# Kernel tuning notes

Hardware: AMD Instinct MI355X
Metric: run time of the kernel (lower is better)

The kernel has to match this reference:

```python
import jax, jax.numpy as jnp
import numpy as np

B, T, IN, OUT = 32, 128, 512, 512
N, Wd, R, H = 128, 64, 4, 512      # memory slots, word size, read heads, controller size
EPS = 1e-6
IFACE = R * Wd + R + Wd + 1 + Wd + Wd + R + 1 + 1 + 3 * R  # DNC interface vector size


def setup_inputs() -> dict:
    key = jax.random.key(0)
    ks = jax.random.split(key, 6)
    s = jnp.float32(0.05)
    lstm_in = IN + R * Wd
    return {
        "input_sequence": jax.random.normal(ks[0], (B, T, IN), jnp.float32),
        "Wx": jax.random.normal(ks[1], (lstm_in, 4 * H), jnp.float32) * s,
        "Wh": jax.random.normal(ks[2], (H, 4 * H), jnp.float32) * s,
        "b_lstm": jnp.zeros((4 * H,), jnp.float32),
        "W_iface": jax.random.normal(ks[3], (H, IFACE), jnp.float32) * s,
        "b_iface": jnp.zeros((IFACE,), jnp.float32),
        "W_out": jax.random.normal(ks[4], (R * Wd + H, OUT), jnp.float32) * s,
        "b_out": jnp.zeros((OUT,), jnp.float32),
    }


def _alloc(u):
    """DNC allocation weighting for one example. u: [N] usage in [0,1]."""
    phi = jnp.argsort(u)                      # ascending usage (data-dependent gather)
    su = u[phi]
    cp = jnp.cumprod(su)
    cp_excl = jnp.concatenate([jnp.ones((1,), su.dtype), cp[:-1]])
    a_sorted = (1.0 - su) * cp_excl
    return jnp.zeros_like(u).at[phi].set(a_sorted)  # scatter back to original order


def _content(M, keys, beta):
    """Cosine content addressing. M: [B,N,W], keys: [B,K,W], beta: [B,K] -> [B,K,N]."""
    Mn = M / (jnp.linalg.norm(M, axis=-1, keepdims=True) + EPS)
    kn = keys / (jnp.linalg.norm(keys, axis=-1, keepdims=True) + EPS)
    sim = jnp.einsum('bnw,bkw->bkn', Mn, kn)
    return jax.nn.softmax(beta[..., None] * sim, axis=-1)


def _dnc_forward(input_sequence, Wx, Wh, b_lstm, W_iface, b_iface, W_out, b_out):
    eye = 1.0 - jnp.eye(N, dtype=jnp.float32)

    def step(carry, x_t):
        h, c, M, usage, link, prec, ww, wr, reads = carry
        # --- LSTM controller ---
        z = jnp.concatenate([x_t, reads], -1) @ Wx + h @ Wh + b_lstm
        i_g, f_g, g_g, o_g = jnp.split(z, 4, axis=-1)
        c_n = jax.nn.sigmoid(f_g) * c + jax.nn.sigmoid(i_g) * jnp.tanh(g_g)
        h_n = jax.nn.sigmoid(o_g) * jnp.tanh(c_n)
        # --- interface vector ---
        v = h_n @ W_iface + b_iface
        o = [0]
        def take(n):
            out = v[:, o[0]:o[0] + n]; o[0] += n; return out
        read_keys = take(R * Wd).reshape(B, R, Wd)
        read_beta = 1.0 + jax.nn.softplus(take(R))
        write_key = take(Wd).reshape(B, 1, Wd)
        write_beta = 1.0 + jax.nn.softplus(take(1))
        erase = jax.nn.sigmoid(take(Wd))
        write_vec = take(Wd)
        free = jax.nn.sigmoid(take(R))
        alloc_g = jax.nn.sigmoid(take(1))
        write_g = jax.nn.sigmoid(take(1))
        modes = jax.nn.softmax(take(3 * R).reshape(B, R, 3), axis=-1)
        # --- usage & allocation ---
        retention = jnp.prod(1.0 - free[:, :, None] * wr, axis=1)          # [B,N]
        usage_n = (usage + ww - usage * ww) * retention
        a = jax.vmap(_alloc)(usage_n)
        # --- write ---
        cw = _content(M, write_key, write_beta)[:, 0, :]                    # [B,N]
        ww_n = write_g * (alloc_g * a + (1.0 - alloc_g) * cw)
        M_n = M * (1.0 - ww_n[:, :, None] * erase[:, None, :]) + ww_n[:, :, None] * write_vec[:, None, :]
        # --- temporal link ---
        link_n = ((1.0 - ww_n[:, :, None] - ww_n[:, None, :]) * link
                  + ww_n[:, :, None] * prec[:, None, :]) * eye
        prec_n = (1.0 - ww_n.sum(-1, keepdims=True)) * prec + ww_n
        # --- read ---
        fw = jnp.einsum('bij,brj->bri', link_n, wr)
        bw = jnp.einsum('bji,brj->bri', link_n, wr)
        cr = _content(M_n, read_keys, read_beta)
        wr_n = modes[:, :, 0:1] * bw + modes[:, :, 1:2] * cr + modes[:, :, 2:3] * fw
        reads_n = jnp.einsum('brn,bnw->brw', wr_n, M_n).reshape(B, R * Wd)
        # --- output projection ---
        out = jnp.concatenate([reads_n, h_n], -1) @ W_out + b_out
        return (h_n, c_n, M_n, usage_n, link_n, prec_n, ww_n, wr_n, reads_n), out

    f32 = jnp.float32
    init = (jnp.zeros((B, H), f32), jnp.zeros((B, H), f32),
            jnp.zeros((B, N, Wd), f32), jnp.zeros((B, N), f32),
            jnp.zeros((B, N, N), f32), jnp.zeros((B, N), f32),
            jnp.zeros((B, N), f32), jnp.zeros((B, R, N), f32),
            jnp.zeros((B, R * Wd), f32))
    _, outs = jax.lax.scan(step, init, jnp.swapaxes(input_sequence, 0, 1))
    return jnp.swapaxes(outs, 0, 1)  # [B, T, OUT]


def reference(input_sequence, Wx, Wh, b_lstm, W_iface, b_iface, W_out, b_out):
    return _dnc_forward(input_sequence, Wx, Wh, b_lstm, W_iface, b_iface, W_out, b_out)
```

## Files before the change

kernel.cpp:

```cpp
#include <hip/hip_runtime.h>
#include <math.h>

#define TT 128
#define ZD 2048
#define IFC 471
#define EPSF 1e-6f
#define MST 66
#define LST 130
#define NBLK 256
#define UHT 24640
#define VHT 15424

#define FSP 16
#define NFLAGS 8192

#define D4(a,b) ((a).x*(b).x + (a).y*(b).y + (a).z*(b).z + (a).w*(b).w)

__device__ __forceinline__ float sig_(float x){ return 1.f/(1.f+expf(-x)); }
__device__ __forceinline__ float sp_(float x){ return fmaxf(x,0.f)+log1pf(expf(-fabsf(x))); }

__device__ __forceinline__ void st1(float* p, float v){
  unsigned u; __builtin_memcpy(&u,&v,4);
  __hip_atomic_store((unsigned*)p, u, __ATOMIC_RELAXED, __HIP_MEMORY_SCOPE_AGENT);
}
__device__ __forceinline__ void st2(float* p, float2 v){
  unsigned long long u; __builtin_memcpy(&u,&v,8);
  __hip_atomic_store((unsigned long long*)p, u, __ATOMIC_RELAXED, __HIP_MEMORY_SCOPE_AGENT);
}

__device__ __forceinline__ void arrive(unsigned* f, unsigned gen){
  __syncthreads();
  if (threadIdx.x == 0)
    __hip_atomic_store(f, gen, __ATOMIC_RELAXED, __HIP_MEMORY_SCOPE_AGENT);
}
__device__ __forceinline__ void wait_ge(const unsigned* f, int n, unsigned gen){
  if (threadIdx.x < 64){
    for (int i = threadIdx.x; i < n; i += 64){
      const unsigned* p = f + (size_t)i*FSP;
      if (__hip_atomic_load(p, __ATOMIC_RELAXED, __HIP_MEMORY_SCOPE_AGENT) >= gen) continue;
      int spins = 0; bool done = false;
      while (spins < 64){
        if (__hip_atomic_load(p, __ATOMIC_RELAXED, __HIP_MEMORY_SCOPE_AGENT) >= gen){ done = true; break; }
        __builtin_amdgcn_s_sleep(1); ++spins;
      }
      if (!done){
        while (__hip_atomic_load(p, __ATOMIC_RELAXED, __HIP_MEMORY_SCOPE_AGENT) < gen)
          __builtin_amdgcn_s_sleep(2);
      }
    }
  }
  __syncthreads();
}

__device__ __forceinline__ unsigned bf16rne(float f){
  unsigned u; __builtin_memcpy(&u,&f,4);
  return (u + 0x7fffu + ((u>>16)&1u)) >> 16;
}
__device__ __forceinline__ float bflo(unsigned w){
  unsigned u = w << 16; float f; __builtin_memcpy(&f,&u,4); return f;
}
__device__ __forceinline__ float bfhi(unsigned w){
  unsigned u = w & 0xffff0000u; float f; __builtin_memcpy(&f,&u,4); return f;
}

__global__ __launch_bounds__(256) void gemm_bias(
    const float* __restrict__ A, const float* __restrict__ B,
    const float* __restrict__ bias, float* __restrict__ C,
    int Nc, int K)
{
  __shared__ float As[16][68];
  __shared__ float Bs[16][68];
  const int tid = threadIdx.x;
  const int bx = blockIdx.x, by = blockIdx.y;
  const int tx = tid & 15, ty = tid >> 4;
  const int am = tid >> 2, ak = (tid & 3) * 4;
  const int bk = tid >> 4, bn = (tid & 15) * 4;
  float acc[4][4] = {};
  const float* Ap = A + (size_t)(by*64+am)*K + ak;
  const float* Bp = B + (size_t)bk*Nc + bx*64 + bn;
  for (int k0 = 0; k0 < K; k0 += 16) {
    float4 av = *(const float4*)Ap; Ap += 16;
    float4 bv = *(const float4*)Bp; Bp += (size_t)16*Nc;
    As[ak+0][am]=av.x; As[ak+1][am]=av.y; As[ak+2][am]=av.z; As[ak+3][am]=av.w;
    *(float4*)&Bs[bk][bn] = bv;
    __syncthreads();
#pragma unroll
    for (int kk = 0; kk < 16; ++kk) {
      float4 a4 = *(const float4*)&As[kk][ty*4];
      float4 b4 = *(const float4*)&Bs[kk][tx*4];
      acc[0][0]+=a4.x*b4.x; acc[0][1]+=a4.x*b4.y; acc[0][2]+=a4.x*b4.z; acc[0][3]+=a4.x*b4.w;
      acc[1][0]+=a4.y*b4.x; acc[1][1]+=a4.y*b4.y; acc[1][2]+=a4.y*b4.z; acc[1][3]+=a4.y*b4.w;
      acc[2][0]+=a4.z*b4.x; acc[2][1]+=a4.z*b4.y; acc[2][2]+=a4.z*b4.z; acc[2][3]+=a4.z*b4.w;
      acc[3][0]+=a4.w*b4.x; acc[3][1]+=a4.w*b4.y; acc[3][2]+=a4.w*b4.z; acc[3][3]+=a4.w*b4.w;
    }
    __syncthreads();
  }
  float4 bb = *(const float4*)(bias + bx*64 + tx*4);
#pragma unroll
  for (int i = 0; i < 4; ++i) {
    float4 o;
    o.x = acc[i][0]+bb.x; o.y = acc[i][1]+bb.y; o.z = acc[i][2]+bb.z; o.w = acc[i][3]+bb.w;
    *(float4*)(C + (size_t)(by*64+ty*4+i)*Nc + bx*64 + tx*4) = o;
  }
}

__global__ __launch_bounds__(256) void gemm_out(
    const float* __restrict__ A, const float* __restrict__ B,
    const float* __restrict__ bias, float* __restrict__ C)
{
  __shared__ float As[16][68];
  __shared__ float Bs[16][68];
  const int tid = threadIdx.x;
  const int bx = blockIdx.x, by = blockIdx.y;
  const int tx = tid & 15, ty = tid >> 4;
  const int am = tid >> 2, ak = (tid & 3) * 4;
  const int bk = tid >> 4, bn = (tid & 15) * 4;
  float acc[4][4] = {};
  const int arow = by*64 + am;
  const float* Ap = A + (size_t)(arow >> 5)*UHT + (size_t)(arow & 31)*768 + ak;
  const float* Bp = B + (size_t)bk*512 + bx*64 + bn;
  for (int k0 = 0; k0 < 768; k0 += 16) {
    float4 av = *(const float4*)Ap; Ap += 16;
    float4 bv = *(const float4*)Bp; Bp += (size_t)16*512;
    As[ak+0][am]=av.x; As[ak+1][am]=av.y; As[ak+2][am]=av.z; As[ak+3][am]=av.w;
    *(float4*)&Bs[bk][bn] = bv;
    __syncthreads();
#pragma unroll
    for (int kk = 0; kk < 16; ++kk) {
      float4 a4 = *(const float4*)&As[kk][ty*4];
      float4 b4 = *(const float4*)&Bs[kk][tx*4];
      acc[0][0]+=a4.x*b4.x; acc[0][1]+=a4.x*b4.y; acc[0][2]+=a4.x*b4.z; acc[0][3]+=a4.x*b4.w;
      acc[1][0]+=a4.y*b4.x; acc[1][1]+=a4.y*b4.y; acc[1][2]+=a4.y*b4.z; acc[1][3]+=a4.y*b4.w;
      acc[2][0]+=a4.z*b4.x; acc[2][1]+=a4.z*b4.y; acc[2][2]+=a4.z*b4.z; acc[2][3]+=a4.z*b4.w;
      acc[3][0]+=a4.w*b4.x; acc[3][1]+=a4.w*b4.y; acc[3][2]+=a4.w*b4.z; acc[3][3]+=a4.w*b4.w;
    }
    __syncthreads();
  }
  float4 bb = *(const float4*)(bias + bx*64 + tx*4);
#pragma unroll
  for (int i = 0; i < 4; ++i) {
    int row = by*64 + ty*4 + i;
    int crow = (row & 31)*128 + (row >> 5);
    float4 o;
    o.x = acc[i][0]+bb.x; o.y = acc[i][1]+bb.y; o.z = acc[i][2]+bb.z; o.w = acc[i][3]+bb.w;
    *(float4*)(C + (size_t)crow*512 + bx*64 + tx*4) = o;
  }
}

#define SL_L    0
#define SL_M    16640
#define SL_V    25088
#define SL_WR   25568
#define SL_FW   26080
#define SL_BW   26592
#define SL_CR   27104
#define SL_USG  27616
#define SL_PRC  27744
#define SL_WW   27872
#define SL_SU   28000
#define SL_CPX  28128
#define SL_MN   28256
#define SL_SW   28384
#define SL_CW   28512
#define SL_RNK  28640
#define SL_MSC  28768
#define SL_ER   28832
#define SL_WV   28896
#define SL_TOT  28960

#define CWI_U  29564
#define CUS_F  34004
#define CZH_F  37092
#define CCS_F  37396
#define CTOT_F 37548

__global__ void init_flags(unsigned* flags) {
  int idx = blockIdx.x*1024 + threadIdx.x;
  if (idx < NFLAGS)
    __hip_atomic_store(&flags[idx], 0u, __ATOMIC_RELAXED, __HIP_MEMORY_SCOPE_AGENT);
}

__global__ __launch_bounds__(1024) void dnc_coop(
    const float* __restrict__ Xproj, const float* __restrict__ Wx,
    const float* __restrict__ Wh, const float* __restrict__ Wif,
    const float* __restrict__ bif,
    float* __restrict__ Uh, float* __restrict__ Vh,
    unsigned* __restrict__ flags)
{
  const int blk = blockIdx.x, tid = threadIdx.x;
  extern __shared__ float sm[];
  const int g = blk & 7;
  const int role = blk >> 3;
  unsigned* FHg = flags + (size_t)g*64*FSP;
  unsigned* FVg = FHg + 28*FSP;
  unsigned* FRg = FHg + 56*FSP;

  if (role < 4) {
    const int eg = g*4 + role;
    float* L   = sm + SL_L;   float* Ms  = sm + SL_M;
    float* v   = sm + SL_V;   float* wr  = sm + SL_WR;
    float* fw  = sm + SL_FW;  float* bw  = sm + SL_BW;
    float* cr  = sm + SL_CR;  float* usg = sm + SL_USG;
    float* prc = sm + SL_PRC; float* ww  = sm + SL_WW;
    float* su  = sm + SL_SU;  float* cpx = sm + SL_CPX;
    float* Mn  = sm + SL_MN;  float* swv = sm + SL_SW;
    float* cw  = sm + SL_CW;  int*   rnk = (int*)(sm + SL_RNK);
    float* msc = sm + SL_MSC; float* er_ = sm + SL_ER; float* wv_ = sm + SL_WV;

    for (int i = tid; i < SL_TOT; i += 1024) sm[i] = 0.f;
    __syncthreads();

    for (int t = 0; t < TT; ++t) {
      wait_ge(FVg, 28, t+1);
      if (tid < IFC) v[tid] = Vh[(size_t)t*VHT + eg*480 + tid];
      __syncthreads();
      if (tid < 128) {
        float ret = 1.f;
#pragma unroll
        for (int r = 0; r < 4; ++r) { float fr = sig_(v[453+r]); ret *= 1.f - fr*wr[r*128+tid]; }
        float u = usg[tid], w_ = ww[tid];
        usg[tid] = (u + w_ - u*w_) * ret;
      } else if (tid < 256) {
        int n = tid - 128; float nk = 0.f, dot = 0.f;
#pragma unroll
        for (int w = 0; w < 64; w += 2) {
          float2 k2 = *(float2*)&v[260+w];
          float2 m2 = *(float2*)&Ms[n*MST+w];
          nk += k2.x*k2.x + k2.y*k2.y; dot += m2.x*k2.x + m2.y*k2.y;
        }
        float beta = 1.f + sp_(v[324]);
        swv[n] = beta * dot / ((Mn[n]+EPSF)*(sqrtf(nk)+EPSF));
      } else if (tid < 260) {
        int r = tid - 256; float s = 0.f;
#pragma unroll
        for (int w = 0; w < 64; w += 4) { float4 k4 = *(float4*)&v[r*64+w]; s += D4(k4,k4); }
        msc[1+r] = sqrtf(s);
      } else if (tid == 260) {
        for (int r = 0; r < 4; ++r) {
          float a0 = v[459+r*3], a1 = v[459+r*3+1], a2 = v[459+r*3+2];
          float mx = fmaxf(a0, fmaxf(a1, a2));
          float e0 = expf(a0-mx), e1 = expf(a1-mx), e2 = expf(a2-mx);
          float dn = e0+e1+e2;
          msc[8+r*3] = e0/dn; msc[8+r*3+1] = e1/dn; msc[8+r*3+2] = e2/dn;
        }
      } else if (tid >= 640 && tid < 704) { int w = tid-640; er_[w] = sig_(v[325+w]); }
      else if (tid >= 704 && tid < 768) { int w = tid-704; wv_[w] = v[389+w]; }
      __syncthreads();
      if (tid < 128) {
        float ui = usg[tid]; int rk = 0;
#pragma unroll
        for (int j = 0; j < 128; j += 4) {
          float4 u4 = *(float4*)&usg[j];
          rk += (u4.x < ui || (u4.x == ui && (j+0) < tid)) ? 1 : 0;
          rk += (u4.y < ui || (u4.y == ui && (j+1) < tid)) ? 1 : 0;
          rk += (u4.z < ui || (u4.z == ui && (j+2) < tid)) ? 1 : 0;
          rk += (u4.w < ui || (u4.w == ui && (j+3) < tid)) ? 1 : 0;
        }
        rnk[tid] = rk; su[rk] = ui;
      } else if (tid < 192) {
        int l = tid - 128;
        float s1 = swv[l], s2 = swv[l+64];
        float m = fmaxf(s1, s2);
#pragma unroll
        for (int o = 32; o > 0; o >>= 1) m = fmaxf(m, __shfl_xor(m, o));
        float e1 = expf(s1-m), e2 = expf(s2-m);
        float dn = e1 + e2;
#pragma unroll
        for (int o = 32; o > 0; o >>= 1) dn += __shfl_xor(dn, o);
        cw[l] = e1/dn; cw[l+64] = e2/dn;
      }
      __syncthreads();
      if (tid < 64) {
        float a0 = su[2*tid], a1 = su[2*tid+1];
        float p = a0*a1, sc = p;
#pragma unroll
        for (int off = 1; off < 64; off <<= 1) {
          float o = __shfl_up(sc, off);
          if ((int)tid >= off) sc *= o;
        }
        float ex = __shfl_up(sc, 1);
        if (tid == 0) ex = 1.f;
        cpx[2*tid] = ex;
        cpx[2*tid+1] = ex*a0;
        float ag = sig_(v[457]), wg = sig_(v[458]);
#pragma unroll
        for (int q = 0; q < 2; ++q) {
          int n = 2*tid + q;
          float a_i = (1.f - usg[n]) * cpx[rnk[n]];
          ww[n] = wg * (ag*a_i + (1.f-ag)*cw[n]);
        }
      }
      __syncthreads();
      {
        int n = tid >> 3, q = tid & 7;
        float wwn = ww[n];
        int w8 = q*8;
#pragma unroll
        for (int gq = 0; gq < 4; ++gq) {
          int w = w8 + gq*2;
          float2 m = *(float2*)&Ms[n*MST+w];
          float2 e2 = *(float2*)&er_[w];
          float2 v2 = *(float2*)&wv_[w];
          m.x = m.x*(1.f - wwn*e2.x) + wwn*v2.x;
          m.y = m.y*(1.f - wwn*e2.y) + wwn*v2.y;
          *(float2*)&Ms[n*MST+w] = m;
        }
        int j16 = q*16;
#pragma unroll
        for (int gq = 0; gq < 8; ++gq) {
          int j = j16 + gq*2;
          float2 lv = *(float2*)&L[n*LST + j];
          float2 p2 = *(float2*)&prc[j];
          float2 w2 = *(float2*)&ww[j];
          lv.x = (1.f - wwn - w2.x)*lv.x + wwn*p2.x;
          lv.y = (1.f - wwn - w2.y)*lv.y + wwn*p2.y;
          int d = n - j;
          if (d == 0) lv.x = 0.f;
          if (d == 1) lv.y = 0.f;
          *(float2*)&L[n*LST + j] = lv;
        }
      }
      __syncthreads();
      if (tid < 64) {
        float s = ww[tid] + ww[tid+64];
#pragma unroll
        for (int o = 32; o > 0; o >>= 1) s += __shfl_xor(s, o);
        if (tid == 0) msc[0] = s;
      } else if (tid < 192) {
        int n = tid - 64; float s = 0.f;
#pragma unroll
        for (int w = 0; w < 64; w += 2) { float2 m = *(float2*)&Ms[n*MST+w]; s += m.x*m.x + m.y*m.y; }
        Mn[n] = sqrtf(s);
      }
      __syncthreads();
      if (tid < 256) {
        int half = tid >> 7, t2 = tid & 127;
        int i0 = (t2 >> 2) * 4, sg = t2 & 3;
        float4 av[4] = {{0,0,0,0},{0,0,0,0},{0,0,0,0},{0,0,0,0}};
        if (half == 0) {
#pragma unroll
          for (int m = 0; m < 8; ++m) {
            int j = sg*4 + m*16;
            float4 w0 = *(float4*)&wr[0*128+j];
            float4 w1 = *(float4*)&wr[1*128+j];
            float4 w2 = *(float4*)&wr[2*128+j];
            float4 w3 = *(float4*)&wr[3*128+j];
#pragma unroll
            for (int k = 0; k < 4; ++k) {
              float2 la = *(float2*)&L[(i0+k)*LST+j];
              float2 lb = *(float2*)&L[(i0+k)*LST+j+2];
              float dv0 = la.x*w0.x + la.y*w0.y + lb.x*w0.z + lb.y*w0.w;
              float dv1 = la.x*w1.x + la.y*w1.y + lb.x*w1.z + lb.y*w1.w;
              float dv2 = la.x*w2.x + la.y*w2.y + lb.x*w2.z + lb.y*w2.w;
              float dv3 = la.x*w3.x + la.y*w3.y + lb.x*w3.z + lb.y*w3.w;
              if (k == 0){ av[0].x+=dv0; av[1].x+=dv1; av[2].x+=dv2; av[3].x+=dv3; }
              if (k == 1){ av[0].y+=dv0; av[1].y+=dv1; av[2].y+=dv2; av[3].y+=dv3; }
              if (k == 2){ av[0].z+=dv0; av[1].z+=dv1; av[2].z+=dv2; av[3].z+=dv3; }
              if (k == 3){ av[0].w+=dv0; av[1].w+=dv1; av[2].w+=dv2; av[3].w+=dv3; }
            }
          }
        } else {
#pragma unroll
          for (int m = 0; m < 32; ++m) {
            int j = sg + m*4;
            float2 la = *(float2*)&L[j*LST + i0];
            float2 lb = *(float2*)&L[j*LST + i0 + 2];
            float w0 = wr[j], w1 = wr[128+j], w2 = wr[256+j], w3 = wr[384+j];
            av[0].x+=w0*la.x; av[0].y+=w0*la.y; av[0].z+=w0*lb.x; av[0].w+=w0*lb.y;
            av[1].x+=w1*la.x; av[1].y+=w1*la.y; av[1].z+=w1*lb.x; av[1].w+=w1*lb.y;
            av[2].x+=w2*la.x; av[2].y+=w2*la.y; av[2].z+=w2*lb.x; av[2].w+=w2*lb.y;
            av[3].x+=w3*la.x; av[3].y+=w3*la.y; av[3].z+=w3*lb.x; av[3].w+=w3*lb.y;
          }
        }
#pragma unroll
        for (int r = 0; r < 4; ++r) {
          av[r].x += __shfl_xor(av[r].x,1); av[r].x += __shfl_xor(av[r].x,2);
          av[r].y += __shfl_xor(av[r].y,1); av[r].y += __shfl_xor(av[r].y,2);
          av[r].z += __shfl_xor(av[r].z,1); av[r].z += __shfl_xor(av[r].z,2);
          av[r].w += __shfl_xor(av[r].w,1); av[r].w += __shfl_xor(av[r].w,2);
        }
        if (sg == 0) {
          float* dst = half ? bw : fw;
#pragma unroll
          for (int r = 0; r < 4; ++r) {
            dst[r*128 + i0+0] = av[r].x; dst[r*128 + i0+1] = av[r].y;
            dst[r*128 + i0+2] = av[r].z; dst[r*128 + i0+3] = av[r].w;
          }
        }
      } else if (tid < 384) {
        int n = tid - 256;
        prc[n] = (1.f - msc[0])*prc[n] + ww[n];
      } else if (tid >= 512) {
        int r = (tid >> 7) & 3, n = tid & 127;
        float dot = 0.f;
#pragma unroll
        for (int w = 0; w < 64; w += 2) {
          float2 m2 = *(float2*)&Ms[n*MST+w];
          float2 k2 = *(float2*)&v[r*64+w];
          dot += m2.x*k2.x + m2.y*k2.y;
        }
        float beta = 1.f + sp_(v[256+r]);
        cr[r*128+n] = beta * dot / ((Mn[n]+EPSF)*(msc[1+r]+EPSF));
      }
      __syncthreads();
      if (tid < 256) {
        int r = tid >> 6, l = tid & 63;
        float s1 = cr[r*128+l], s2 = cr[r*128+l+64];
        float m = fmaxf(s1, s2);
#pragma unroll
        for (int o = 32; o > 0; o >>= 1) m = fmaxf(m, __shfl_xor(m, o));
        float e1 = expf(s1-m), e2 = expf(s2-m);
        float dn = e1 + e2;
#pragma unroll
        for (int o = 32; o > 0; o >>= 1) dn += __shfl_xor(dn, o);
        float m0 = msc[8+r*3], m1 = msc[8+r*3+1], m2 = msc[8+r*3+2];
        wr[r*128+l]    = m0*bw[r*128+l]    + m1*(e1/dn) + m2*fw[r*128+l];
        wr[r*128+l+64] = m0*bw[r*128+l+64] + m1*(e2/dn) + m2*fw[r*128+l+64];
      }
      __syncthreads();
      if (tid < 512) {
        int r = tid >> 7, t2 = tid & 127;
        int w0 = (t2 >> 3) * 4, ns = t2 & 7;
        float4 a = {0,0,0,0};
#pragma unroll
        for (int m = 0; m < 16; ++m) {
          int n = ns + m*8;
          float2 ma = *(float2*)&Ms[n*MST + w0];
          float2 mb = *(float2*)&Ms[n*MST + w0 + 2];
          float wv = wr[r*128 + n];
          a.x += wv*ma.x; a.y += wv*ma.y; a.z += wv*mb.x; a.w += wv*mb.y;
        }
        a.x += __shfl_xor(a.x,1); a.x += __shfl_xor(a.x,2); a.x += __shfl_xor(a.x,4);
        a.y += __shfl_xor(a.y,1); a.y += __shfl_xor(a.y,2); a.y += __shfl_xor(a.y,4);
        a.z += __shfl_xor(a.z,1); a.z += __shfl_xor(a.z,2); a.z += __shfl_xor(a.z,4);
        a.w += __shfl_xor(a.w,1); a.w += __shfl_xor(a.w,2); a.w += __shfl_xor(a.w,4);
        if (ns == 0) {
          int o = r*64 + w0;
          float2 lo = {a.x, a.y}, hi = {a.z, a.w};
          st2(&Uh[(size_t)t*UHT + eg*768 + o], lo);
          st2(&Uh[(size_t)t*UHT + eg*768 + o + 2], hi);
        }
      }
      arrive(&FRg[role*FSP], t+1);
    }
  } else {
    const int c = role - 4;
    const int egB = g*4;
    const int d0 = (512*c)/28, d1 = (512*(c+1))/28, Dd = d1-d0, NJ = 4*Dd;
    const int v0 = (471*c)/28, v1 = (471*(c+1))/28, JV = v1-v0;
    unsigned* Wzu = (unsigned*)sm;
    unsigned* Wiu = (unsigned*)sm + CWI_U;
    float* us  = sm + CUS_F;
    float* zh  = sm + CZH_F;
    float* cst = sm + CCS_F;

    for (int idx = tid; idx < NJ*384; idx += 1024) {
      int j = idx/384, p = idx - j*384, k = 2*p;
      int q = j/Dd, di = j - q*Dd, gc = q*512 + d0 + di;
      float w0 = (k < 256) ? Wx[(size_t)(512+k)*ZD + gc] : Wh[(size_t)(k-256)*ZD + gc];
      float w1 = (k+1 < 256) ? Wx[(size_t)(513+k)*ZD + gc] : Wh[(size_t)(k-255)*ZD + gc];
      Wzu[j*389 + p] = bf16rne(w0) | (bf16rne(w1) << 16);
    }
    for (int idx = tid; idx < JV*256; idx += 1024) {
      int j = idx/256, p = idx - j*256, k = 2*p, gc = v0 + j;
      float w0 = Wif[(size_t)k*IFC + gc];
      float w1 = Wif[(size_t)(k+1)*IFC + gc];
      Wiu[j*261 + p] = bf16rne(w0) | (bf16rne(w1) << 16);
    }
    if (tid < 76) cst[tid] = 0.f;
    if (tid < 4*NJ) {
      int e = tid/NJ, j = tid - e*NJ;
      int q = j/Dd, di = j - q*Dd, gc = q*512 + d0 + di;
      zh[e*76 + j] = Xproj[((size_t)(egB+e)*TT + 0)*ZD + gc];
    }
    __syncthreads();
    if (tid < 4*Dd) {
      int e = tid/Dd, di = tid - e*Dd;
      float zi = zh[e*76 + di], zg = zh[e*76 + 2*Dd + di], zo = zh[e*76 + 3*Dd + di];
      float cn = sig_(zi)*tanhf(zg);
      float hn = sig_(zo)*tanhf(cn);
      cst[tid] = cn;
      st1(&Uh[(size_t)0*UHT + (egB + e)*768 + 256 + d0 + di], hn);
    }
    arrive(&FHg[c*FSP], 1);

    for (int t = 0; t < TT; ++t) {
      float xpre = 0.f; int pe = 0, pj = 0;
      if (t+1 < TT && tid < 4*NJ) {
        pe = tid/NJ; pj = tid - pe*NJ;
        int q = pj/Dd, di = pj - q*Dd, gc = q*512 + d0 + di;
        xpre = Xproj[((size_t)(egB+pe)*TT + t+1)*ZD + gc];
      }
      wait_ge(FHg, 28, t+1);
      if (tid < 512) {
        int e = tid >> 7, f4 = (tid & 127) * 4;
        *(float4*)&us[e*772 + 256 + f4] =
            *(const float4*)&Uh[(size_t)t*UHT + (egB+e)*768 + 256 + f4];
      }
      if (t+1 < TT && tid < 4*NJ) {
        zh[pe*76 + pj] = xpre;
      }
      __syncthreads();
      if (tid < 544) {
        int g8 = tid >> 3, ks = tid & 7;
        int e = g8/17, j = g8 - e*17;
        if (j < JV) {
          float acc = 0.f;
#pragma unroll 4
          for (int m = 0; m < 32; ++m) {
            int p = m*8 + ks;
            float2 hv = *(const float2*)&us[e*772 + 256 + 2*p];
            unsigned wu = Wiu[j*261 + p];
            acc += hv.x*bflo(wu) + hv.y*bfhi(wu);
          }
          acc += __shfl_xor(acc,1); acc += __shfl_xor(acc,2); acc += __shfl_xor(acc,4);
          if (ks == 0) {
            int col = v0 + j;
            st1(&Vh[(size_t)t*VHT + (egB+e)*480 + col], bif[col] + acc);
          }
        }
      }
      arrive(&FVg[c*FSP], t+1);
      if (t+1 < TT) {
        if (tid < 608) {
          int q2 = tid >> 1, ks = tid & 1;
          int e = q2/76, j = q2 - e*76;
          if (j < NJ) {
            float acc = 0.f;
#pragma unroll 4
            for (int m = 0; m < 128; ++m) {
              int pp = m*2 + ks;
              float2 hv = *(const float2*)&us[e*772 + 256 + 2*pp];
              unsigned wu = Wzu[j*389 + 128 + pp];
              acc += hv.x*bflo(wu) + hv.y*bfhi(wu);
            }
            acc += __shfl_xor(acc,1);
            if (ks == 0) zh[e*76 + j] += acc;
          }
        }
        wait_ge(FRg, 4, t+1);
        if (tid < 256) {
          int e = tid >> 6, f4 = (tid & 63) * 4;
          *(float4*)&us[e*772 + f4] =
              *(const float4*)&Uh[(size_t)t*UHT + (egB+e)*768 + f4];
        }
        __syncthreads();
        if (tid < 608) {
          int q2 = tid >> 1, ks = tid & 1;
          int e = q2/76, j = q2 - e*76;
          if (j < NJ) {
            float acc = 0.f;
#pragma unroll 4
            for (int m = 0; m < 64; ++m) {
              int pp = m*2 + ks;
              float2 rv = *(const float2*)&us[e*772 + 2*pp];
              unsigned wu = Wzu[j*389 + pp];
              acc += rv.x*bflo(wu) + rv.y*bfhi(wu);
            }
            acc += __shfl_xor(acc,1);
            if (ks == 0) zh[e*76 + j] += acc;
          }
        }
        __syncthreads();
        if (tid < 4*Dd) {
          int e = tid/Dd, di = tid - e*Dd;
          float zi = zh[e*76 + di],      zf = zh[e*76 + Dd + di];
          float zg = zh[e*76 + 2*Dd+di], zo = zh[e*76 + 3*Dd + di];
          float cn = sig_(zf)*cst[tid] + sig_(zi)*tanhf(zg);
          float hn = sig_(zo)*tanhf(cn);
          cst[tid] = cn;
          st1(&Uh[(size_t)(t+1)*UHT + (egB+e)*768 + 256 + d0 + di], hn);
        }
        arrive(&FHg[c*FSP], t+2);
      }
    }
  }
}

extern "C" void kernel_launch(void* const* d_in, const int* in_sizes, int n_in,
                              void* d_out, int out_size, void* d_ws, size_t ws_size,
                              hipStream_t stream) {
  const float* x   = (const float*)d_in[0];
  const float* Wx  = (const float*)d_in[1];
  const float* Wh  = (const float*)d_in[2];
  const float* bl  = (const float*)d_in[3];
  const float* Wif = (const float*)d_in[4];
  const float* bif = (const float*)d_in[5];
  const float* Wo  = (const float*)d_in[6];
  const float* bo  = (const float*)d_in[7];
  float* out = (float*)d_out;

  unsigned* fl = (unsigned*)d_ws;
  float* Xp = (float*)(fl + NFLAGS);
  float* Uh = Xp + (size_t)4096*2048;
  float* Vh = Uh + (size_t)TT*UHT;

  gemm_bias<<<dim3(2048/64, 4096/64), dim3(256), 0, stream>>>(x, Wx, bl, Xp, 2048, 512);

  init_flags<<<dim3(8), dim3(1024), 0, stream>>>(fl);

  const int smem_bytes = CTOT_F * 4;
  (void)hipFuncSetAttribute((const void*)dnc_coop, hipFuncAttributeMaxDynamicSharedMemorySize, smem_bytes);
  void* args[] = { (void*)&Xp, (void*)&Wx, (void*)&Wh, (void*)&Wif, (void*)&bif,
                   (void*)&Uh, (void*)&Vh, (void*)&fl };
  (void)hipLaunchCooperativeKernel((void*)dnc_coop, dim3(NBLK), dim3(1024), args,
                                   (unsigned int)smem_bytes, stream);

  gemm_out<<<dim3(512/64, 4096/64), dim3(256), 0, stream>>>(Uh, Wo, bo, out);
}
```

Measured before the change: 4.112 ms.

## Fuse interface projection into LSTM step via split-K partial sums

Each controller block now computes its slice of h right after the LSTM cell and immediately multiplies it by the matching rows of W_iface, writing split-K partial interface vectors. The memory blocks sum the 28 partials plus bias. This removes one full grid-sync round (waiting for all h before computing the interface) from the critical path per timestep. The cost is 28x more global reads on the memory-side blocks and a Vpart buffer that is reused across timesteps, which relies on the flag ordering to avoid overwriting partials that have not yet been read.

```diff
diff --git a/kernel.cpp b/kernel.cpp
--- a/kernel.cpp
+++ b/kernel.cpp
@@ -9,7 +9,6 @@
 #define LST 130
 #define NBLK 256
 #define UHT 24640
-#define VHT 15424
 
 #define FSP 16
 #define NFLAGS 8192
@@ -26,6 +25,10 @@
 __device__ __forceinline__ void st2(float* p, float2 v){
   unsigned long long u; __builtin_memcpy(&u,&v,8);
   __hip_atomic_store((unsigned long long*)p, u, __ATOMIC_RELAXED, __HIP_MEMORY_SCOPE_AGENT);
+}
+__device__ __forceinline__ float ld1(const float* p){
+  unsigned u = __hip_atomic_load((const unsigned*)p, __ATOMIC_RELAXED, __HIP_MEMORY_SCOPE_AGENT);
+  float f; __builtin_memcpy(&f,&u,4); return f;
 }
 
 __device__ __forceinline__ void arrive(unsigned* f, unsigned gen){
@@ -167,12 +170,18 @@
 #define SL_ER   28832
 #define SL_WV   28896
 #define SL_TOT  28960
-
-#define CWI_U  29564
-#define CUS_F  34004
-#define CZH_F  37092
-#define CCS_F  37396
-#define CTOT_F 37548
+#define SL_BIF  28960
+
+#define CWR_U  29564
+#define CUS_F  34067
+#define CZH_F  37155
+#define CCS_F  37459
+#define CHS_F  37539
+#define CTOT_F 37619
+
+#define VPE 480
+#define VPC (4*VPE)
+#define VPG (28*VPC)
 
 __global__ void init_flags(unsigned* flags) {
   int idx = blockIdx.x*1024 + threadIdx.x;
@@ -184,7 +193,7 @@
     const float* __restrict__ Xproj, const float* __restrict__ Wx,
     const float* __restrict__ Wh, const float* __restrict__ Wif,
     const float* __restrict__ bif,
-    float* __restrict__ Uh, float* __restrict__ Vh,
+    float* __restrict__ Uh, float* __restrict__ Vpart,
     unsigned* __restrict__ flags)
 {
   const int blk = blockIdx.x, tid = threadIdx.x;
@@ -206,13 +215,22 @@
     float* Mn  = sm + SL_MN;  float* swv = sm + SL_SW;
     float* cw  = sm + SL_CW;  int*   rnk = (int*)(sm + SL_RNK);
     float* msc = sm + SL_MSC; float* er_ = sm + SL_ER; float* wv_ = sm + SL_WV;
+    float* bifs= sm + SL_BIF;
+    const float* Vp = Vpart + (size_t)g*VPG + (size_t)role*VPE;
 
     for (int i = tid; i < SL_TOT; i += 1024) sm[i] = 0.f;
+    if (tid < IFC) bifs[tid] = bif[tid];
     __syncthreads();
 
     for (int t = 0; t < TT; ++t) {
       wait_ge(FVg, 28, t+1);
-      if (tid < IFC) v[tid] = Vh[(size_t)t*VHT + eg*480 + tid];
+      if (tid < IFC) {
+        float s = bifs[tid];
+#pragma unroll 7
+        for (int cc = 0; cc < 28; ++cc)
+          s += ld1(Vp + (size_t)cc*VPC + tid);
+        v[tid] = s;
+      }
       __syncthreads();
       if (tid < 128) {
         float ret = 1.f;
@@ -447,12 +465,13 @@
     const int c = role - 4;
     const int egB = g*4;
     const int d0 = (512*c)/28, d1 = (512*(c+1))/28, Dd = d1-d0, NJ = 4*Dd;
-    const int v0 = (471*c)/28, v1 = (471*(c+1))/28, JV = v1-v0;
-    unsigned* Wzu = (unsigned*)sm;
-    unsigned* Wiu = (unsigned*)sm + CWI_U;
+    unsigned* Wzu  = (unsigned*)sm;
+    unsigned* WifR = (unsigned*)sm + CWR_U;
     float* us  = sm + CUS_F;
     float* zh  = sm + CZH_F;
     float* cst = sm + CCS_F;
+    float* hsl = sm + CHS_F;
+    float* Vpc = Vpart + (size_t)g*VPG + (size_t)c*VPC;
 
     for (int idx = tid; idx < NJ*384; idx += 1024) {
       int j = idx/384, p = idx - j*384, k = 2*p;
@@ -461,13 +480,14 @@
       float w1 = (k+1 < 256) ? Wx[(size_t)(513+k)*ZD + gc] : Wh[(size_t)(k-255)*ZD + gc];
       Wzu[j*389 + p] = bf16rne(w0) | (bf16rne(w1) << 16);
     }
-    for (int idx = tid; idx < JV*256; idx += 1024) {
-      int j = idx/256, p = idx - j*256, k = 2*p, gc = v0 + j;
-      float w0 = Wif[(size_t)k*IFC + gc];
-      float w1 = Wif[(size_t)(k+1)*IFC + gc];
-      Wiu[j*261 + p] = bf16rne(w0) | (bf16rne(w1) << 16);
-    }
-    if (tid < 76) cst[tid] = 0.f;
+    for (int idx = tid; idx < Dd*236; idx += 1024) {
+      int di = idx/236, p = idx - di*236;
+      int c0 = 2*p, c1 = 2*p+1;
+      float w0 = Wif[(size_t)(d0+di)*IFC + c0];
+      float w1 = (c1 < IFC) ? Wif[(size_t)(d0+di)*IFC + c1] : 0.f;
+      WifR[di*237 + p] = bf16rne(w0) | (bf16rne(w1) << 16);
+    }
+    if (tid < 80) cst[tid] = 0.f;
     if (tid < 4*NJ) {
       int e = tid/NJ, j = tid - e*NJ;
       int q = j/Dd, di = j - q*Dd, gc = q*512 + d0 + di;
@@ -480,13 +500,26 @@
       float cn = sig_(zi)*tanhf(zg);
       float hn = sig_(zo)*tanhf(cn);
       cst[tid] = cn;
+      hsl[e*20 + di] = hn;
       st1(&Uh[(size_t)0*UHT + (egB + e)*768 + 256 + d0 + di], hn);
     }
+    __syncthreads();
+    if (tid < 944) {
+      int e = tid/236, jp = tid - e*236;
+      float2 acc = {0.f, 0.f};
+      for (int di = 0; di < Dd; ++di) {
+        float hh = hsl[e*20 + di];
+        unsigned wu = WifR[di*237 + jp];
+        acc.x += hh*bflo(wu); acc.y += hh*bfhi(wu);
+      }
+      st2(&Vpc[(size_t)e*VPE + 2*jp], acc);
+    }
+    arrive(&FVg[c*FSP], 1);
     arrive(&FHg[c*FSP], 1);
 
-    for (int t = 0; t < TT; ++t) {
+    for (int t = 0; t < TT-1; ++t) {
       float xpre = 0.f; int pe = 0, pj = 0;
-      if (t+1 < TT && tid < 4*NJ) {
+      if (tid < 4*NJ) {
         pe = tid/NJ; pj = tid - pe*NJ;
         int q = pj/Dd, di = pj - q*Dd, gc = q*512 + d0 + di;
         xpre = Xproj[((size_t)(egB+pe)*TT + t+1)*ZD + gc];
@@ -497,82 +530,71 @@
         *(float4*)&us[e*772 + 256 + f4] =
             *(const float4*)&Uh[(size_t)t*UHT + (egB+e)*768 + 256 + f4];
       }
-      if (t+1 < TT && tid < 4*NJ) {
-        zh[pe*76 + pj] = xpre;
-      }
-      __syncthreads();
-      if (tid < 544) {
-        int g8 = tid >> 3, ks = tid & 7;
-        int e = g8/17, j = g8 - e*17;
-        if (j < JV) {
+      if (tid < 4*NJ) zh[pe*76 + pj] = xpre;
+      __syncthreads();
+      if (tid < 608) {
+        int q2 = tid >> 1, ks = tid & 1;
+        int e = q2/76, j = q2 - e*76;
+        if (j < NJ) {
           float acc = 0.f;
 #pragma unroll 4
-          for (int m = 0; m < 32; ++m) {
-            int p = m*8 + ks;
-            float2 hv = *(const float2*)&us[e*772 + 256 + 2*p];
-            unsigned wu = Wiu[j*261 + p];
+          for (int m = 0; m < 128; ++m) {
+            int pp = m*2 + ks;
+            float2 hv = *(const float2*)&us[e*772 + 256 + 2*pp];
+            unsigned wu = Wzu[j*389 + 128 + pp];
             acc += hv.x*bflo(wu) + hv.y*bfhi(wu);
           }
-          acc += __shfl_xor(acc,1); acc += __shfl_xor(acc,2); acc += __shfl_xor(acc,4);
-          if (ks == 0) {
-            int col = v0 + j;
-            st1(&Vh[(size_t)t*VHT + (egB+e)*480 + col], bif[col] + acc);
+          acc += __shfl_xor(acc,1);
+          if (ks == 0) zh[e*76 + j] += acc;
+        }
+      }
+      wait_ge(FRg, 4, t+1);
+      if (tid < 256) {
+        int e = tid >> 6, f4 = (tid & 63) * 4;
+        *(float4*)&us[e*772 + f4] =
+            *(const float4*)&Uh[(size_t)t*UHT + (egB+e)*768 + f4];
+      }
+      __syncthreads();
+      if (tid < 608) {
+        int q2 = tid >> 1, ks = tid & 1;
+        int e = q2/76, j = q2 - e*76;
+        if (j < NJ) {
+          float acc = 0.f;
+#pragma unroll 4
+          for (int m = 0; m < 64; ++m) {
+            int pp = m*2 + ks;
+            float2 rv = *(const float2*)&us[e*772 + 2*pp];
+            unsigned wu = Wzu[j*389 + pp];
+            acc += rv.x*bflo(wu) + rv.y*bfhi(wu);
           }
-        }
-      }
-      arrive(&FVg[c*FSP], t+1);
-      if (t+1 < TT) {
-        if (tid < 608) {
-          int q2 = tid >> 1, ks = tid & 1;
-          int e = q2/76, j = q2 - e*76;
-          if (j < NJ) {
-            float acc = 0.f;
-#pragma unroll 4
-            for (int m = 0; m < 128; ++m) {
-              int pp = m*2 + ks;
-              float2 hv = *(const float2*)&us[e*772 + 256 + 2*pp];
-              unsigned wu = Wzu[j*389 + 128 + pp];
-              acc += hv.x*bflo(wu) + hv.y*bfhi(wu);
-            }
-            acc += __shfl_xor(acc,1);
-            if (ks == 0) zh[e*76 + j] += acc;
-          }
-        }
-        wait_ge(FRg, 4, t+1);
-        if (tid < 256) {
-          int e = tid >> 6, f4 = (tid & 63) * 4;
-          *(float4*)&us[e*772 + f4] =
-              *(const float4*)&Uh[(size_t)t*UHT + (egB+e)*768 + f4];
-        }
-        __syncthreads();
-        if (tid < 608) {
-          int q2 = tid >> 1, ks = tid & 1;
-          int e = q2/76, j = q2 - e*76;
-          if (j < NJ) {
-            float acc = 0.f;
-#pragma unroll 4
-            for (int m = 0; m < 64; ++m) {
-              int pp = m*2 + ks;
-              float2 rv = *(const float2*)&us[e*772 + 2*pp];
-              unsigned wu = Wzu[j*389 + pp];
-              acc += rv.x*bflo(wu) + rv.y*bfhi(wu);
-            }
-            acc += __shfl_xor(acc,1);
-            if (ks == 0) zh[e*76 + j] += acc;
-          }
-        }
-        __syncthreads();
-        if (tid < 4*Dd) {
-          int e = tid/Dd, di = tid - e*Dd;
-          float zi = zh[e*76 + di],      zf = zh[e*76 + Dd + di];
-          float zg = zh[e*76 + 2*Dd+di], zo = zh[e*76 + 3*Dd + di];
-          float cn = sig_(zf)*cst[tid] + sig_(zi)*tanhf(zg);
-          float hn = sig_(zo)*tanhf(cn);
-          cst[tid] = cn;
-          st1(&Uh[(size_t)(t+1)*UHT + (egB+e)*768 + 256 + d0 + di], hn);
-        }
-        arrive(&FHg[c*FSP], t+2);
-      }
+          acc += __shfl_xor(acc,1);
+          if (ks == 0) zh[e*76 + j] += acc;
+        }
+      }
+      __syncthreads();
+      if (tid < 4*Dd) {
+        int e = tid/Dd, di = tid - e*Dd;
+        float zi = zh[e*76 + di],      zf = zh[e*76 + Dd + di];
+        float zg = zh[e*76 + 2*Dd+di], zo = zh[e*76 + 3*Dd + di];
+        float cn = sig_(zf)*cst[tid] + sig_(zi)*tanhf(zg);
+        float hn = sig_(zo)*tanhf(cn);
+        cst[tid] = cn;
+        hsl[e*20 + di] = hn;
+        st1(&Uh[(size_t)(t+1)*UHT + (egB+e)*768 + 256 + d0 + di], hn);
+      }
+      __syncthreads();
+      if (tid < 944) {
+        int e = tid/236, jp = tid - e*236;
+        float2 acc = {0.f, 0.f};
+        for (int di = 0; di < Dd; ++di) {
+          float hh = hsl[e*20 + di];
+          unsigned wu = WifR[di*237 + jp];
+          acc.x += hh*bflo(wu); acc.y += hh*bfhi(wu);
+        }
+        st2(&Vpc[(size_t)e*VPE + 2*jp], acc);
+      }
+      arrive(&FVg[c*FSP], t+2);
+      arrive(&FHg[c*FSP], t+2);
     }
   }
 }
@@ -593,7 +615,7 @@
   unsigned* fl = (unsigned*)d_ws;
   float* Xp = (float*)(fl + NFLAGS);
   float* Uh = Xp + (size_t)4096*2048;
-  float* Vh = Uh + (size_t)TT*UHT;
+  float* Vpart = Uh + (size_t)TT*UHT;
 
   gemm_bias<<<dim3(2048/64, 4096/64), dim3(256), 0, stream>>>(x, Wx, bl, Xp, 2048, 512);
 
@@ -602,7 +624,7 @@
   const int smem_bytes = CTOT_F * 4;
   (void)hipFuncSetAttribute((const void*)dnc_coop, hipFuncAttributeMaxDynamicSharedMemorySize, smem_bytes);
   void* args[] = { (void*)&Xp, (void*)&Wx, (void*)&Wh, (void*)&Wif, (void*)&bif,
-                   (void*)&Uh, (void*)&Vh, (void*)&fl };
+                   (void*)&Uh, (void*)&Vpart, (void*)&fl };
   (void)hipLaunchCooperativeKernel((void*)dnc_coop, dim3(NBLK), dim3(1024), args,
                                    (unsigned int)smem_bytes, stream);
 
```

New measurement: 7.497 ms. 82.3% more time.
